# Kernel tuning notes

Measured on AMD Instinct MI355X. Metric: run time of the kernel, lower is better.

## Reference

```python
import jax, jax.numpy as jnp
import numpy as np

H = 256   # hidden_size
L = 6     # num_layers
IN = 128  # input_size
B = 128   # batch
T = 512   # seq_len


def setup_inputs() -> dict:
    key = jax.random.key(0)
    ks = jax.random.split(key, 9)
    s = 1.0 / np.sqrt(H)  # PyTorch LSTM init: U(-1/sqrt(H), 1/sqrt(H))
    x = jax.random.normal(ks[0], (B, T, IN), jnp.float32)
    h0 = jax.random.normal(ks[1], (L, B, H), jnp.float32)
    c0 = jax.random.normal(ks[2], (L, B, H), jnp.float32)
    w_ih0 = jax.random.uniform(ks[3], (4 * H, IN), jnp.float32, -s, s)
    w_ih = jax.random.uniform(ks[4], (L - 1, 4 * H, H), jnp.float32, -s, s)
    w_hh = jax.random.uniform(ks[5], (L, 4 * H, H), jnp.float32, -s, s)
    b_ih = jax.random.uniform(ks[6], (L, 4 * H), jnp.float32, -s, s)
    b_hh = jax.random.uniform(ks[7], (L, 4 * H), jnp.float32, -s, s)
    return {"x": x, "h0": h0, "c0": c0, "w_ih0": w_ih0, "w_ih": w_ih,
            "w_hh": w_hh, "b_ih": b_ih, "b_hh": b_hh}


def _lstm_layer(x, h0, c0, w_ih, w_hh, b):
    """One unidirectional LSTM layer. x: [B,T,Din] -> outputs [B,T,H], (hT, cT)."""
    # Precompute input contribution for all timesteps at once: [B,T,4H]
    xg = jnp.einsum('btd,gd->btg', x, w_ih) + b

    def step(carry, g_t):
        h, c = carry
        g = g_t + h @ w_hh.T  # [B,4H]
        i, f, gc, o = jnp.split(g, 4, axis=-1)  # PyTorch gate order i,f,g,o
        i = jax.nn.sigmoid(i)
        f = jax.nn.sigmoid(f)
        o = jax.nn.sigmoid(o)
        gc = jnp.tanh(gc)
        c = f * c + i * gc
        h = o * jnp.tanh(c)
        return (h, c), h

    (hT, cT), ys = jax.lax.scan(step, (h0, c0), jnp.swapaxes(xg, 0, 1))
    return jnp.swapaxes(ys, 0, 1), hT, cT


def reference(x, h0, c0, w_ih0, w_ih, w_hh, b_ih, b_hh):
    # Stacked 6-layer LSTM; fc / noop linear in the original is dead code.
    # Original returns state[0] (final hidden states, [L,B,H]) as float32.
    hs = []
    inp = x
    for l in range(L):
        wih_l = w_ih0 if l == 0 else w_ih[l - 1]
        b_l = b_ih[l] + b_hh[l]
        inp, hT, _ = _lstm_layer(inp, h0[l], c0[l], wih_l, w_hh[l], b_l)
        hs.append(hT)
    return jnp.stack(hs).astype(jnp.float32)  # [L, B, H]
```

## Files before the change

kernel.cpp:

```cpp
#include <hip/hip_runtime.h>

#define NLAYER 6
#define NB     128
#define NT     512
#define DIN    128
#define NH     256
#define NBLK   192
#define TSLOT_U64 (NB*NH/2)

typedef __attribute__((ext_vector_type(8))) short short8;
typedef __attribute__((ext_vector_type(4))) float f32x4;
typedef unsigned long long u64;

__device__ __forceinline__ unsigned f2bf2(float lo, float hi){
  unsigned a = __float_as_uint(lo), b = __float_as_uint(hi);
  a = (a + 0x7fffu + ((a>>16)&1u)) >> 16;
  b = (b + 0x7fffu + ((b>>16)&1u)) >> 16;
  return a | (b<<16);
}
__device__ __forceinline__ u64 f2bf4(float a, float b, float c, float d){
  return (u64)f2bf2(a,b) | ((u64)f2bf2(c,d) << 32);
}
__device__ __forceinline__ short8 pack16(u64 lo, u64 hi){
  union { u64 u[2]; short8 v; } w; w.u[0]=lo; w.u[1]=hi; return w.v;
}
__device__ __forceinline__ short8 ld8f_frag(const float* p){
  f32x4 a = *(const f32x4*)p;
  f32x4 b = *(const f32x4*)(p+4);
  return pack16(f2bf4(a[0],a[1],a[2],a[3]), f2bf4(b[0],b[1],b[2],b[3]));
}

__device__ __forceinline__ float sigmf(float v){ return 1.0f/(1.0f + __expf(-v)); }
__device__ __forceinline__ float tanhfast(float v){
  v = fminf(fmaxf(v, -15.0f), 15.0f);
  float e = __expf(2.0f*v);
  return (e - 1.0f)/(e + 1.0f);
}

__device__ __forceinline__ int ld_flag(const int* p){
  return __hip_atomic_load(p, __ATOMIC_RELAXED, __HIP_MEMORY_SCOPE_AGENT);
}
__device__ __forceinline__ void st_flag(int* p, int v){
  __hip_atomic_store(p, v, __ATOMIC_RELAXED, __HIP_MEMORY_SCOPE_AGENT);
}
__device__ __forceinline__ u64 ring_ld(const u64* p){
  return __hip_atomic_load(p, __ATOMIC_RELAXED, __HIP_MEMORY_SCOPE_AGENT);
}
__device__ __forceinline__ void ring_st(u64* p, u64 v){
  __hip_atomic_store(p, v, __ATOMIC_RELAXED, __HIP_MEMORY_SCOPE_AGENT);
}

__device__ __forceinline__ unsigned tagw(float f, unsigned tag){
  unsigned a = __float_as_uint(f);
  return ((a + 0x7fffu + ((a>>16)&1u)) & 0xffff0000u) | tag;
}
__device__ __forceinline__ unsigned strip2(u64 q){
  return __builtin_amdgcn_perm((unsigned)(q>>32), (unsigned)q, 0x07060302u);
}

__device__ __forceinline__ short8 lds_frag(const unsigned* __restrict__ buf, int row, int soff){
  return *(const short8*)((const short*)buf + row*264 + soff);
}

template<int NKX>
__device__ __forceinline__ void lstm_run(
    const float* __restrict__ x,  const float* __restrict__ h0,
    const float* __restrict__ c0, const float* __restrict__ wx,
    const float* __restrict__ wh, const float* __restrict__ bi,
    const float* __restrict__ bh, float* __restrict__ out,
    int* __restrict__ acks, u64* __restrict__ ring, unsigned (*ldsb)[2112],
    int Wv, int l, int bg, int s, int wv, int lane)
{
  constexpr int KIT  = NKX + 8;
  constexpr int KX   = NKX*32;
  constexpr bool HASX = (NKX == 8);
  const int l15  = lane & 15;
  const int quad = lane >> 4;
  const int bloc = bg*16 + l15;
  const int jcol = s*16 + quad*4;
  const int Wm   = Wv - 1;

  short8 A[4][KIT];
  #pragma unroll
  for (int q = 0; q < 4; ++q){
    const float* wrow_x = wx + (size_t)(q*NH + s*16 + l15)*KX;
    const float* wrow_h = wh + (size_t)(q*NH + s*16 + l15)*NH;
    #pragma unroll
    for (int kt = 0; kt < KIT; ++kt){
      int k0 = kt*32 + quad*8;
      A[q][kt] = (k0 < KX) ? ld8f_frag(wrow_x + k0)
                           : ld8f_frag(wrow_h + (k0 - KX));
    }
  }

  f32x4 bsv[4];
  #pragma unroll
  for (int q = 0; q < 4; ++q){
    f32x4 a = *(const f32x4*)(bi + q*NH + jcol);
    f32x4 b = *(const f32x4*)(bh + q*NH + jcol);
    bsv[q] = a + b;
  }
  float cc[4];
  {
    f32x4 cv = *(const f32x4*)(c0 + ((size_t)l*NB + bloc)*NH + jcol);
    cc[0]=cv[0]; cc[1]=cv[1]; cc[2]=cv[2]; cc[3]=cv[3];
  }

  const int* ackOwn = acks + (l*8 + bg)*16;
  int* ackPrevW = HASX ? acks + ((l-1)*8 + bg)*16 + s : nullptr;
  const u64* ringPrev = HASX ? ring + (size_t)(l-1)*Wv*TSLOT_U64 : nullptr;
  u64*       ringOwn  = ring + (size_t)l*Wv*TSLOT_U64;
  const bool lastL = (l == NLAYER-1);
  const bool wrap  = (Wv < NT);
  int ackmin = 0;

  const int sbase = wv*512 + lane*2;

  for (int t = 0; t < NT; ++t){
    const int slot  = t & Wm;
    const int pslot = (t-1) & Wm;

    if (wrap && !lastL && t >= Wv){
      const int need = t - Wv + 1;
      if (ackmin < need){
        int v = 0, guard = 0;
        for (;;){
          v = (lane < 16) ? ld_flag(ackOwn + lane) : 0x7fffffff;
          if (__ballot(v >= need) == ~0ull) break;
          __builtin_amdgcn_s_sleep(1);
          if (++guard > (1<<22)) break;
        }
        int m = v;
        #pragma unroll
        for (int o = 8; o; o >>= 1) m = min(m, __shfl_xor(m, o));
        ackmin = __shfl(m, 0);
      }
    }

    short8 Bx[NKX];
    if constexpr (!HASX){
      const float* px = x + ((size_t)bloc*NT + t)*DIN + quad*8;
      #pragma unroll
      for (int k = 0; k < NKX; ++k) Bx[k] = ld8f_frag(px + k*32);
    }

    const u64* srcX = HASX ? ringPrev + (size_t)slot*TSLOT_U64 + bg*2048 : nullptr;
    const u64* srcH = (t > 0) ? ringOwn + (size_t)pslot*TSLOT_U64 + bg*2048 : nullptr;
    unsigned* ldsX = ldsb[(t&1)*2 + 0];
    unsigned* ldsH = ldsb[(t&1)*2 + 1];
    u64 qx[8], qh[8];
    {
      bool okx = !HASX, okh = (srcH == nullptr);
      const u64 tx2 = (u64)(unsigned)(t+1) * 0x0000000100000001ull;
      const u64 th2 = (u64)(unsigned)t     * 0x0000000100000001ull;
      int guard = 0;
      while (!(okx & okh)){
        if (!okx){
          #pragma unroll
          for (int c = 0; c < 4; ++c){
            qx[c*2]   = ring_ld(srcX + sbase + c*128);
            qx[c*2+1] = ring_ld(srcX + sbase + c*128 + 1);
          }
        }
        if (!okh){
          #pragma unroll
          for (int c = 0; c < 4; ++c){
            qh[c*2]   = ring_ld(srcH + sbase + c*128);
            qh[c*2+1] = ring_ld(srcH + sbase + c*128 + 1);
          }
        }
        if (!okx){
          u64 m = 0;
          #pragma unroll
          for (int i = 0; i < 8; ++i) m |= qx[i] ^ tx2;
          okx = (__ballot(((unsigned)(m | (m>>32)) & 0xffffu) == 0u) == ~0ull);
        }
        if (!okh){
          u64 m = 0;
          #pragma unroll
          for (int i = 0; i < 8; ++i) m |= qh[i] ^ th2;
          okh = (__ballot(((unsigned)(m | (m>>32)) & 0xffffu) == 0u) == ~0ull);
        }
        if (okx & okh) break;
        __builtin_amdgcn_s_sleep(1);
        if (++guard > (1<<20)) break;
      }
    }
    if constexpr (HASX){
      #pragma unroll
      for (int c = 0; c < 4; ++c)
        *(u64*)(ldsX + (wv*4+c)*132 + lane*2) =
            (u64)strip2(qx[c*2]) | ((u64)strip2(qx[c*2+1]) << 32);
    }
    if (srcH){
      #pragma unroll
      for (int c = 0; c < 4; ++c)
        *(u64*)(ldsH + (wv*4+c)*132 + lane*2) =
            (u64)strip2(qh[c*2]) | ((u64)strip2(qh[c*2+1]) << 32);
    }
    __syncthreads();

    if (HASX && wrap && ((t & 7) == 7) && lane == 0) st_flag(ackPrevW, t+1);

    if constexpr (HASX){
      #pragma unroll
      for (int k = 0; k < NKX; ++k) Bx[k] = lds_frag(ldsX, l15, quad*8 + k*32);
    }
    short8 Bh[8];
    if (t == 0){
      const float* ph = h0 + ((size_t)l*NB + bloc)*NH + quad*8;
      #pragma unroll
      for (int k = 0; k < 8; ++k) Bh[k] = ld8f_frag(ph + k*32);
    } else {
      #pragma unroll
      for (int k = 0; k < 8; ++k) Bh[k] = lds_frag(ldsH, l15, quad*8 + k*32);
    }

    f32x4 a0 = {0,0,0,0}, a1 = {0,0,0,0}, a2 = {0,0,0,0}, a3 = {0,0,0,0};
    #pragma unroll
    for (int k = 0; k < NKX; ++k){
      a0 = __builtin_amdgcn_mfma_f32_16x16x32_bf16(A[0][k], Bx[k], a0, 0, 0, 0);
      a1 = __builtin_amdgcn_mfma_f32_16x16x32_bf16(A[1][k], Bx[k], a1, 0, 0, 0);
      a2 = __builtin_amdgcn_mfma_f32_16x16x32_bf16(A[2][k], Bx[k], a2, 0, 0, 0);
      a3 = __builtin_amdgcn_mfma_f32_16x16x32_bf16(A[3][k], Bx[k], a3, 0, 0, 0);
    }
    #pragma unroll
    for (int k = 0; k < 8; ++k){
      a0 = __builtin_amdgcn_mfma_f32_16x16x32_bf16(A[0][NKX+k], Bh[k], a0, 0, 0, 0);
      a1 = __builtin_amdgcn_mfma_f32_16x16x32_bf16(A[1][NKX+k], Bh[k], a1, 0, 0, 0);
      a2 = __builtin_amdgcn_mfma_f32_16x16x32_bf16(A[2][NKX+k], Bh[k], a2, 0, 0, 0);
      a3 = __builtin_amdgcn_mfma_f32_16x16x32_bf16(A[3][NKX+k], Bh[k], a3, 0, 0, 0);
    }

    float hv[4];
    #pragma unroll
    for (int r = 0; r < 4; ++r){
      float ig = sigmf(a0[r] + bsv[0][r]);
      float fg = sigmf(a1[r] + bsv[1][r]);
      float gv = tanhfast(a2[r] + bsv[2][r]);
      float og = sigmf(a3[r] + bsv[3][r]);
      float cn = fg*cc[r] + ig*gv;
      cc[r] = cn;
      hv[r] = og * tanhfast(cn);
    }

    u64* hp = ringOwn + (size_t)slot*TSLOT_U64 + (size_t)bloc*128 + s*8 + quad*2;
    const unsigned otag = (unsigned)(t+1);
    ring_st(hp,     (u64)tagw(hv[0], otag) | ((u64)tagw(hv[1], otag) << 32));
    ring_st(hp + 1, (u64)tagw(hv[2], otag) | ((u64)tagw(hv[3], otag) << 32));
    if (t == NT-1){
      f32x4 ov; ov[0]=hv[0]; ov[1]=hv[1]; ov[2]=hv[2]; ov[3]=hv[3];
      *(f32x4*)(out + ((size_t)l*NB + bloc)*NH + jcol) = ov;
    }
  }
}

__global__ __launch_bounds__(256, 1)
void lstm_pipe(const float* __restrict__ x,   const float* __restrict__ h0,
               const float* __restrict__ c0,  const float* __restrict__ wih0,
               const float* __restrict__ wih, const float* __restrict__ whh,
               const float* __restrict__ bih, const float* __restrict__ bhh,
               float* __restrict__ out, int* __restrict__ acks,
               u64* __restrict__ ring, int Wv)
{
  __shared__ unsigned ldsb[4][2112];
  const int bid  = blockIdx.x;
  const int bg   = bid & 7;
  const int j    = bid >> 3;
  const int l    = j >> 2;
  const int b    = j & 3;
  const int lane = threadIdx.x & 63;
  const int wv   = threadIdx.x >> 6;
  const int s    = b*4 + wv;

  if (l == 0)
    lstm_run<4>(x, h0, c0, wih0, whh, bih, bhh,
                out, acks, ring, ldsb, Wv, 0, bg, s, wv, lane);
  else
    lstm_run<8>(x, h0, c0,
                wih + (size_t)(l-1)*(4*NH*NH),
                whh + (size_t)l*(4*NH*NH),
                bih + (size_t)l*(4*NH),
                bhh + (size_t)l*(4*NH),
                out, acks, ring, ldsb, Wv, l, bg, s, wv, lane);
}

extern "C" void kernel_launch(void* const* d_in, const int* in_sizes, int n_in,
                              void* d_out, int out_size, void* d_ws, size_t ws_size,
                              hipStream_t stream)
{
  (void)in_sizes; (void)n_in; (void)out_size;
  const float* x    = (const float*)d_in[0];
  const float* h0   = (const float*)d_in[1];
  const float* c0   = (const float*)d_in[2];
  const float* wih0 = (const float*)d_in[3];
  const float* wih  = (const float*)d_in[4];
  const float* whh  = (const float*)d_in[5];
  const float* bih  = (const float*)d_in[6];
  const float* bhh  = (const float*)d_in[7];

  int Wv = 32;
  size_t ringB;
  for (;;){
    ringB = (size_t)NLAYER*Wv*TSLOT_U64*8;
    if (8192 + ringB <= ws_size || Wv <= 8) break;
    Wv >>= 1;
  }

  int* acks = (int*)d_ws;
  u64* ring = (u64*)((char*)d_ws + 8192);

  (void)hipMemsetAsync(d_ws, 0, 8192 + ringB, stream);
  hipLaunchKernelGGL(lstm_pipe, dim3(NBLK), dim3(256), 0, stream,
                     x, h0, c0, wih0, wih, whh, bih, bhh,
                     (float*)d_out, acks, ring, Wv);
}
```

Before: 2.091 ms.

## Split x/h polling so input MFMAs overlap recurrent wait; use cache-bypass asm ring I/O

Polling for the previous layer's input and for the own-layer recurrent h are split into separate stages. The x-part MFMAs are issued before waiting on h, so input-projection work overlaps the recurrent dependency latency. Ring loads and stores become inline-asm dwordx4 ops with sc0/sc1 cache bits, and the store is issued twice to publish data. The LDS pitch changes to 70 u64, likely to avoid bank conflicts. The changes add a second __syncthreads per step, drop the sleep in the spin loop, and rely on hand-picked cache-coherence bits.

Result: slower. 3.129 ms (+49.7%).

```diff
diff --git a/kernel.cpp b/kernel.cpp
--- a/kernel.cpp
+++ b/kernel.cpp
@@ -7,9 +7,11 @@
 #define NH     256
 #define NBLK   192
 #define TSLOT_U64 (NB*NH/2)
+#define LPITCH64  70
 
 typedef __attribute__((ext_vector_type(8))) short short8;
 typedef __attribute__((ext_vector_type(4))) float f32x4;
+typedef __attribute__((ext_vector_type(4))) unsigned uint4v;
 typedef unsigned long long u64;
 
 __device__ __forceinline__ unsigned f2bf2(float lo, float hi){
@@ -43,12 +45,6 @@
 __device__ __forceinline__ void st_flag(int* p, int v){
   __hip_atomic_store(p, v, __ATOMIC_RELAXED, __HIP_MEMORY_SCOPE_AGENT);
 }
-__device__ __forceinline__ u64 ring_ld(const u64* p){
-  return __hip_atomic_load(p, __ATOMIC_RELAXED, __HIP_MEMORY_SCOPE_AGENT);
-}
-__device__ __forceinline__ void ring_st(u64* p, u64 v){
-  __hip_atomic_store(p, v, __ATOMIC_RELAXED, __HIP_MEMORY_SCOPE_AGENT);
-}
 
 __device__ __forceinline__ unsigned tagw(float f, unsigned tag){
   unsigned a = __float_as_uint(f);
@@ -58,8 +54,61 @@
   return __builtin_amdgcn_perm((unsigned)(q>>32), (unsigned)q, 0x07060302u);
 }
 
-__device__ __forceinline__ short8 lds_frag(const unsigned* __restrict__ buf, int row, int soff){
-  return *(const short8*)((const short*)buf + row*264 + soff);
+__device__ __forceinline__ void ld4x16_sc0(const u64* base, uint4v q[4]){
+  asm volatile(
+    "global_load_dwordx4 %0, %4, off sc0\n\t"
+    "global_load_dwordx4 %1, %4, off offset:1024 sc0\n\t"
+    "global_load_dwordx4 %2, %4, off offset:2048 sc0\n\t"
+    "global_load_dwordx4 %3, %4, off offset:3072 sc0\n\t"
+    "s_waitcnt vmcnt(0)"
+    : "=&v"(q[0]), "=&v"(q[1]), "=&v"(q[2]), "=&v"(q[3])
+    : "v"(base) : "memory");
+}
+__device__ __forceinline__ void ld4x16_sc01(const u64* base, uint4v q[4]){
+  asm volatile(
+    "global_load_dwordx4 %0, %4, off sc0 sc1\n\t"
+    "global_load_dwordx4 %1, %4, off offset:1024 sc0 sc1\n\t"
+    "global_load_dwordx4 %2, %4, off offset:2048 sc0 sc1\n\t"
+    "global_load_dwordx4 %3, %4, off offset:3072 sc0 sc1\n\t"
+    "s_waitcnt vmcnt(0)"
+    : "=&v"(q[0]), "=&v"(q[1]), "=&v"(q[2]), "=&v"(q[3])
+    : "v"(base) : "memory");
+}
+__device__ __forceinline__ void st16_pub(u64* p, uint4v v){
+  asm volatile(
+    "global_store_dwordx4 %0, %1, off sc0 sc1\n\t"
+    "global_store_dwordx4 %0, %1, off sc0"
+    :: "v"(p), "v"(v) : "memory");
+}
+
+__device__ __forceinline__ void poll_stage(const u64* __restrict__ src, unsigned tag,
+                                           u64* __restrict__ ldsPlane, int wv, int lane){
+  const u64* base = src + (size_t)wv*512 + (size_t)lane*2;
+  uint4v q[4];
+  int it = 0, guard = 0;
+  for (;;){
+    ++it;
+    if (it > 3 && (it & 1)) ld4x16_sc01(base, q);
+    else                    ld4x16_sc0(base, q);
+    unsigned bad = 0;
+    #pragma unroll
+    for (int c = 0; c < 4; ++c){
+      uint4v xq = q[c] ^ tag;
+      bad |= xq[0] | xq[1] | xq[2] | xq[3];
+    }
+    if (__ballot((bad & 0xffffu) == 0u) == ~0ull) break;
+    if (++guard > (1<<22)) break;
+  }
+  u64* lp = ldsPlane + (size_t)(wv*4)*LPITCH64 + lane;
+  #pragma unroll
+  for (int c = 0; c < 4; ++c){
+    union { uint4v v; u64 d[2]; } uq; uq.v = q[c];
+    lp[c*LPITCH64] = (u64)strip2(uq.d[0]) | ((u64)strip2(uq.d[1]) << 32);
+  }
+}
+
+__device__ __forceinline__ short8 lds_frag(const u64* __restrict__ buf, int row, int soff){
+  return *(const short8*)((const short*)buf + row*280 + soff);
 }
 
 template<int NKX>
@@ -68,7 +117,7 @@
     const float* __restrict__ c0, const float* __restrict__ wx,
     const float* __restrict__ wh, const float* __restrict__ bi,
     const float* __restrict__ bh, float* __restrict__ out,
-    int* __restrict__ acks, u64* __restrict__ ring, unsigned (*ldsb)[2112],
+    int* __restrict__ acks, u64* __restrict__ ring, u64 (*ldsb)[16*LPITCH64],
     int Wv, int l, int bg, int s, int wv, int lane)
 {
   constexpr int KIT  = NKX + 8;
@@ -113,8 +162,6 @@
   const bool lastL = (l == NLAYER-1);
   const bool wrap  = (Wv < NT);
   int ackmin = 0;
-
-  const int sbase = wv*512 + lane*2;
 
   for (int t = 0; t < NT; ++t){
     const int slot  = t & Wm;
@@ -137,92 +184,42 @@
       }
     }
 
+    u64* ldsX = ldsb[(t&1)*2 + 0];
+    u64* ldsH = ldsb[(t&1)*2 + 1];
     short8 Bx[NKX];
-    if constexpr (!HASX){
+    if constexpr (HASX){
+      poll_stage(ringPrev + (size_t)slot*TSLOT_U64 + bg*2048, (unsigned)(t+1),
+                 ldsX, wv, lane);
+      __syncthreads();
+      if (wrap && ((t & 7) == 7) && lane == 0) st_flag(ackPrevW, t+1);
+      #pragma unroll
+      for (int k = 0; k < NKX; ++k) Bx[k] = lds_frag(ldsX, l15, quad*8 + k*32);
+    } else {
       const float* px = x + ((size_t)bloc*NT + t)*DIN + quad*8;
       #pragma unroll
       for (int k = 0; k < NKX; ++k) Bx[k] = ld8f_frag(px + k*32);
     }
 
-    const u64* srcX = HASX ? ringPrev + (size_t)slot*TSLOT_U64 + bg*2048 : nullptr;
-    const u64* srcH = (t > 0) ? ringOwn + (size_t)pslot*TSLOT_U64 + bg*2048 : nullptr;
-    unsigned* ldsX = ldsb[(t&1)*2 + 0];
-    unsigned* ldsH = ldsb[(t&1)*2 + 1];
-    u64 qx[8], qh[8];
-    {
-      bool okx = !HASX, okh = (srcH == nullptr);
-      const u64 tx2 = (u64)(unsigned)(t+1) * 0x0000000100000001ull;
-      const u64 th2 = (u64)(unsigned)t     * 0x0000000100000001ull;
-      int guard = 0;
-      while (!(okx & okh)){
-        if (!okx){
-          #pragma unroll
-          for (int c = 0; c < 4; ++c){
-            qx[c*2]   = ring_ld(srcX + sbase + c*128);
-            qx[c*2+1] = ring_ld(srcX + sbase + c*128 + 1);
-          }
-        }
-        if (!okh){
-          #pragma unroll
-          for (int c = 0; c < 4; ++c){
-            qh[c*2]   = ring_ld(srcH + sbase + c*128);
-            qh[c*2+1] = ring_ld(srcH + sbase + c*128 + 1);
-          }
-        }
-        if (!okx){
-          u64 m = 0;
-          #pragma unroll
-          for (int i = 0; i < 8; ++i) m |= qx[i] ^ tx2;
-          okx = (__ballot(((unsigned)(m | (m>>32)) & 0xffffu) == 0u) == ~0ull);
-        }
-        if (!okh){
-          u64 m = 0;
-          #pragma unroll
-          for (int i = 0; i < 8; ++i) m |= qh[i] ^ th2;
-          okh = (__ballot(((unsigned)(m | (m>>32)) & 0xffffu) == 0u) == ~0ull);
-        }
-        if (okx & okh) break;
-        __builtin_amdgcn_s_sleep(1);
-        if (++guard > (1<<20)) break;
-      }
-    }
-    if constexpr (HASX){
-      #pragma unroll
-      for (int c = 0; c < 4; ++c)
-        *(u64*)(ldsX + (wv*4+c)*132 + lane*2) =
-            (u64)strip2(qx[c*2]) | ((u64)strip2(qx[c*2+1]) << 32);
-    }
-    if (srcH){
-      #pragma unroll
-      for (int c = 0; c < 4; ++c)
-        *(u64*)(ldsH + (wv*4+c)*132 + lane*2) =
-            (u64)strip2(qh[c*2]) | ((u64)strip2(qh[c*2+1]) << 32);
-    }
-    __syncthreads();
-
-    if (HASX && wrap && ((t & 7) == 7) && lane == 0) st_flag(ackPrevW, t+1);
-
-    if constexpr (HASX){
-      #pragma unroll
-      for (int k = 0; k < NKX; ++k) Bx[k] = lds_frag(ldsX, l15, quad*8 + k*32);
-    }
+    f32x4 a0 = {0,0,0,0}, a1 = {0,0,0,0}, a2 = {0,0,0,0}, a3 = {0,0,0,0};
+    #pragma unroll
+    for (int k = 0; k < NKX; ++k){
+      a0 = __builtin_amdgcn_mfma_f32_16x16x32_bf16(A[0][k], Bx[k], a0, 0, 0, 0);
+      a1 = __builtin_amdgcn_mfma_f32_16x16x32_bf16(A[1][k], Bx[k], a1, 0, 0, 0);
+      a2 = __builtin_amdgcn_mfma_f32_16x16x32_bf16(A[2][k], Bx[k], a2, 0, 0, 0);
+      a3 = __builtin_amdgcn_mfma_f32_16x16x32_bf16(A[3][k], Bx[k], a3, 0, 0, 0);
+    }
+
     short8 Bh[8];
     if (t == 0){
       const float* ph = h0 + ((size_t)l*NB + bloc)*NH + quad*8;
       #pragma unroll
       for (int k = 0; k < 8; ++k) Bh[k] = ld8f_frag(ph + k*32);
     } else {
+      poll_stage(ringOwn + (size_t)pslot*TSLOT_U64 + bg*2048, (unsigned)t,
+                 ldsH, wv, lane);
+      __syncthreads();
       #pragma unroll
       for (int k = 0; k < 8; ++k) Bh[k] = lds_frag(ldsH, l15, quad*8 + k*32);
-    }
-
-    f32x4 a0 = {0,0,0,0}, a1 = {0,0,0,0}, a2 = {0,0,0,0}, a3 = {0,0,0,0};
-    #pragma unroll
-    for (int k = 0; k < NKX; ++k){
-      a0 = __builtin_amdgcn_mfma_f32_16x16x32_bf16(A[0][k], Bx[k], a0, 0, 0, 0);
-      a1 = __builtin_amdgcn_mfma_f32_16x16x32_bf16(A[1][k], Bx[k], a1, 0, 0, 0);
-      a2 = __builtin_amdgcn_mfma_f32_16x16x32_bf16(A[2][k], Bx[k], a2, 0, 0, 0);
-      a3 = __builtin_amdgcn_mfma_f32_16x16x32_bf16(A[3][k], Bx[k], a3, 0, 0, 0);
     }
     #pragma unroll
     for (int k = 0; k < 8; ++k){
@@ -244,10 +241,13 @@
       hv[r] = og * tanhfast(cn);
     }
 
-    u64* hp = ringOwn + (size_t)slot*TSLOT_U64 + (size_t)bloc*128 + s*8 + quad*2;
-    const unsigned otag = (unsigned)(t+1);
-    ring_st(hp,     (u64)tagw(hv[0], otag) | ((u64)tagw(hv[1], otag) << 32));
-    ring_st(hp + 1, (u64)tagw(hv[2], otag) | ((u64)tagw(hv[3], otag) << 32));
+    {
+      const unsigned otag = (unsigned)(t+1);
+      uint4v pv;
+      pv[0] = tagw(hv[0], otag); pv[1] = tagw(hv[1], otag);
+      pv[2] = tagw(hv[2], otag); pv[3] = tagw(hv[3], otag);
+      st16_pub(ringOwn + (size_t)slot*TSLOT_U64 + (size_t)bloc*128 + s*8 + quad*2, pv);
+    }
     if (t == NT-1){
       f32x4 ov; ov[0]=hv[0]; ov[1]=hv[1]; ov[2]=hv[2]; ov[3]=hv[3];
       *(f32x4*)(out + ((size_t)l*NB + bloc)*NH + jcol) = ov;
@@ -263,7 +263,7 @@
                float* __restrict__ out, int* __restrict__ acks,
                u64* __restrict__ ring, int Wv)
 {
-  __shared__ unsigned ldsb[4][2112];
+  __shared__ u64 ldsb[4][16*LPITCH64];
   const int bid  = blockIdx.x;
   const int bg   = bid & 7;
   const int j    = bid >> 3;
```
